# Kernel tuning notes

Hardware: AMD Instinct MI355X
Metric: run time of the kernel (lower is better)

The kernel has to match this reference:

```python
import jax, jax.numpy as jnp
import numpy as np

B, S, H = 8, 2048, 768      # batch, seq_len, hidden_size
N = 512                     # spans per example
MAXW = 30                   # max span width (length in [0, MAXW-1] -> width <= MAXW)


def setup_inputs() -> dict:
    key = jax.random.key(0)
    k1, k2, k3, k4 = jax.random.split(key, 4)
    embeddings = jax.random.normal(k1, (B, S, H), dtype=jnp.float32)
    starts = jax.random.randint(k2, (B, N), 0, S - MAXW)          # span starts
    lengths = jax.random.randint(k3, (B, N), 0, MAXW)             # end = start + length
    w = jax.random.normal(k4, (H, 1), dtype=jnp.float32) * 0.02   # nn.Linear(hidden, 1) weight (transposed)
    b = jnp.zeros((1,), dtype=jnp.float32)                        # linear bias
    return {"embeddings": embeddings, "w": w, "b": b, "starts": starts, "lengths": lengths}


def reference(embeddings, w, b, starts, lengths):
    # Vectorized ragged span pooling: gather up to MAXW tokens per span,
    # masked softmax over attention scores, then concat [start, end, attn].
    ends = starts + lengths                                  # inclusive end index
    offs = jnp.arange(MAXW)                                  # (W,)
    positions = starts[..., None] + offs                     # (B, N, W)
    mask = offs[None, None, :] <= lengths[..., None]         # (B, N, W) valid-token mask

    gather = jax.vmap(lambda e, p: e[p])                     # per-example gather
    span_emb = gather(embeddings, positions)                 # (B, N, W, H)

    scores = span_emb @ w + b                                # (B, N, W, 1)
    scores = jnp.where(mask[..., None], scores, -jnp.inf)
    attn_w = jax.nn.softmax(scores, axis=2)                  # masked softmax over span width
    attn_out = jnp.sum(attn_w * span_emb, axis=2)            # (B, N, H)

    start_emb = gather(embeddings, starts)                   # (B, N, H)
    end_emb = gather(embeddings, ends)                       # (B, N, H)
    return jnp.concatenate([start_emb, end_emb, attn_out], axis=-1)  # (B, N, 3H)
```

## Files before the change

### kernel.cpp

```cpp
#include <hip/hip_runtime.h>
#include <hip/hip_bf16.h>
#include <math.h>

#define BB 8
#define SS 2048
#define HH 768
#define NN 512
#define MAXW 30

__global__ __launch_bounds__(256) void sort_spans_kernel(
    const int* __restrict__ starts,
    int*       __restrict__ order)
{
    const int b   = blockIdx.x;
    const int tid = threadIdx.x;
    __shared__ int hist[SS];
    __shared__ int wsum[4];

    for (int i = tid; i < SS; i += 256) hist[i] = 0;
    __syncthreads();

    const int* st = starts + b * NN;
    for (int n = tid; n < NN; n += 256) atomicAdd(&hist[st[n]], 1);
    __syncthreads();

    const int base = tid * 8;
    int cnt[8]; int s = 0;
    #pragma unroll
    for (int k = 0; k < 8; ++k) { cnt[k] = hist[base + k]; s += cnt[k]; }

    const int lane = tid & 63, wv = tid >> 6;
    int v = s;
    #pragma unroll
    for (int off = 1; off < 64; off <<= 1) {
        int u = __shfl_up(v, off);
        if (lane >= off) v += u;
    }
    if (lane == 63) wsum[wv] = v;
    __syncthreads();
    int wbase = 0;
    #pragma unroll
    for (int k = 0; k < 4; ++k) wbase += (k < wv) ? wsum[k] : 0;

    int excl = wbase + v - s;
    #pragma unroll
    for (int k = 0; k < 8; ++k) { int c = cnt[k]; hist[base + k] = excl; excl += c; }
    __syncthreads();

    for (int n = tid; n < NN; n += 256) {
        int pos = atomicAdd(&hist[st[n]], 1);
        order[b * NN + pos] = n;
    }
}

__global__ __launch_bounds__(256) void span_fused_kernel(
    const float* __restrict__ emb,
    const float* __restrict__ w,
    const float* __restrict__ bias,
    const int*   __restrict__ starts,
    const int*   __restrict__ lengths,
    const int*   __restrict__ order,
    float*       __restrict__ out)
{
    const int tid  = threadIdx.x;
    const int wv   = tid >> 6;
    const int lane = tid & 63;
    const int bi   = blockIdx.x & 7;
    const int rank = ((int)blockIdx.x >> 3) * 4 + wv;
    const int n    = order ? order[bi * NN + rank] : rank;
    const int span = bi * NN + n;

    const int start = starts[span];
    const int len   = lengths[span];

    const float* ebase = emb + (size_t)bi * SS * HH + (size_t)start * HH;
    const int h0 = lane * 4;
    float* orow = out + (size_t)span * (3 * HH);

    const float4 w0 = *reinterpret_cast<const float4*>(w + h0);
    const float4 w1 = *reinterpret_cast<const float4*>(w + h0 + 256);
    const float4 w2 = *reinterpret_cast<const float4*>(w + h0 + 512);
    const float bb = bias[0];

    float m = -INFINITY, ssum = 0.f;
    float4 a0 = make_float4(0.f, 0.f, 0.f, 0.f), a1 = a0, a2 = a0;

    const float* row = ebase;
    float4 v0 = *reinterpret_cast<const float4*>(row + h0);
    float4 v1 = *reinterpret_cast<const float4*>(row + h0 + 256);
    float4 v2 = *reinterpret_cast<const float4*>(row + h0 + 512);

    for (int t = 0; t <= len; ++t) {
        float4 n0, n1, n2;
        if (t < len) {
            const float* nr = row + HH;
            n0 = *reinterpret_cast<const float4*>(nr + h0);
            n1 = *reinterpret_cast<const float4*>(nr + h0 + 256);
            n2 = *reinterpret_cast<const float4*>(nr + h0 + 512);
        }

        float d = v0.x * w0.x + v0.y * w0.y + v0.z * w0.z + v0.w * w0.w
                + v1.x * w1.x + v1.y * w1.y + v1.z * w1.z + v1.w * w1.w
                + v2.x * w2.x + v2.y * w2.y + v2.z * w2.z + v2.w * w2.w;
        #pragma unroll
        for (int off = 32; off; off >>= 1) d += __shfl_xor(d, off);
        d += bb;

        if (d > m) {
            const float c = __expf(m - d);
            ssum *= c;
            a0.x *= c; a0.y *= c; a0.z *= c; a0.w *= c;
            a1.x *= c; a1.y *= c; a1.z *= c; a1.w *= c;
            a2.x *= c; a2.y *= c; a2.z *= c; a2.w *= c;
            m = d;
        }
        const float pt = __expf(d - m);
        ssum += pt;
        a0.x += pt * v0.x; a0.y += pt * v0.y; a0.z += pt * v0.z; a0.w += pt * v0.w;
        a1.x += pt * v1.x; a1.y += pt * v1.y; a1.z += pt * v1.z; a1.w += pt * v1.w;
        a2.x += pt * v2.x; a2.y += pt * v2.y; a2.z += pt * v2.z; a2.w += pt * v2.w;

        if (t == 0) {
            *reinterpret_cast<float4*>(orow + h0)       = v0;
            *reinterpret_cast<float4*>(orow + h0 + 256) = v1;
            *reinterpret_cast<float4*>(orow + h0 + 512) = v2;
        }
        if (t == len) {
            *reinterpret_cast<float4*>(orow + HH + h0)       = v0;
            *reinterpret_cast<float4*>(orow + HH + h0 + 256) = v1;
            *reinterpret_cast<float4*>(orow + HH + h0 + 512) = v2;
        }

        v0 = n0; v1 = n1; v2 = n2;
        row += HH;
    }

    const float inv = 1.f / ssum;
    a0.x *= inv; a0.y *= inv; a0.z *= inv; a0.w *= inv;
    a1.x *= inv; a1.y *= inv; a1.z *= inv; a1.w *= inv;
    a2.x *= inv; a2.y *= inv; a2.z *= inv; a2.w *= inv;
    *reinterpret_cast<float4*>(orow + 2 * HH + h0)       = a0;
    *reinterpret_cast<float4*>(orow + 2 * HH + h0 + 256) = a1;
    *reinterpret_cast<float4*>(orow + 2 * HH + h0 + 512) = a2;
}

extern "C" void kernel_launch(void* const* d_in, const int* in_sizes, int n_in,
                              void* d_out, int out_size, void* d_ws, size_t ws_size,
                              hipStream_t stream) {
    const float* emb     = (const float*)d_in[0];
    const float* w       = (const float*)d_in[1];
    const float* bias    = (const float*)d_in[2];
    const int*   starts  = (const int*)d_in[3];
    const int*   lengths = (const int*)d_in[4];
    float*       out     = (float*)d_out;

    int* order = nullptr;
    if (ws_size >= (size_t)(BB * NN * sizeof(int))) {
        order = (int*)d_ws;
        sort_spans_kernel<<<dim3(BB), dim3(256), 0, stream>>>(starts, order);
    }

    span_fused_kernel<<<dim3(BB * NN / 4), dim3(256), 0, stream>>>(
        emb, w, bias, starts, lengths, order, out);
}
```

Measured before the change: 31.79 us.

## Share token rows across 8 sorted spans via double-buffered LDS chunks

Each 512-thread block now handles 8 start-sorted spans. It loads the union token window cooperatively in chunks of 8 rows into double-buffered shared memory, computing each row's score once. Each wave then runs the online softmax for its own span using the shared rows and scores. The aim is to remove redundant global loads and dot products for overlapping spans, at the cost of block-wide barriers, LDS traffic and possible loads of tokens no span in the block needs when the spans are spread apart.

New measurement: 36.76 us. +15.6%, slower.

```diff
diff --git a/kernel.cpp b/kernel.cpp
--- a/kernel.cpp
+++ b/kernel.cpp
@@ -7,6 +7,8 @@
 #define HH 768
 #define NN 512
 #define MAXW 30
+#define SPW 8
+#define CH  8
 
 __global__ __launch_bounds__(256) void sort_spans_kernel(
     const int* __restrict__ starts,
@@ -53,7 +55,7 @@
     }
 }
 
-__global__ __launch_bounds__(256) void span_fused_kernel(
+__global__ __launch_bounds__(512, 4) void span_block_kernel(
     const float* __restrict__ emb,
     const float* __restrict__ w,
     const float* __restrict__ bias,
@@ -66,73 +68,117 @@
     const int wv   = tid >> 6;
     const int lane = tid & 63;
     const int bi   = blockIdx.x & 7;
-    const int rank = ((int)blockIdx.x >> 3) * 4 + wv;
+    const int g    = (int)blockIdx.x >> 3;
+    const int rank = g * SPW + wv;
     const int n    = order ? order[bi * NN + rank] : rank;
     const int span = bi * NN + n;
 
     const int start = starts[span];
     const int len   = lengths[span];
-
-    const float* ebase = emb + (size_t)bi * SS * HH + (size_t)start * HH;
+    const int end   = start + len;
+
+    __shared__ float s_rows[2][CH][HH];
+    __shared__ float s_scr[2][CH];
+    __shared__ int   s_s[SPW], s_e[SPW];
+
+    if (lane == 0) { s_s[wv] = start; s_e[wv] = end; }
+    __syncthreads();
+    int wlo = s_s[0], whi = s_e[0];
+    #pragma unroll
+    for (int k = 1; k < SPW; ++k) { wlo = min(wlo, s_s[k]); whi = max(whi, s_e[k]); }
+
     const int h0 = lane * 4;
-    float* orow = out + (size_t)span * (3 * HH);
-
+    const float* ebase = emb + (size_t)bi * SS * HH;
     const float4 w0 = *reinterpret_cast<const float4*>(w + h0);
     const float4 w1 = *reinterpret_cast<const float4*>(w + h0 + 256);
     const float4 w2 = *reinterpret_cast<const float4*>(w + h0 + 512);
     const float bb = bias[0];
 
+    const int nch = (whi - wlo) / CH + 1;
+
+    auto produce = [&](int c) {
+        const int tok = wlo + c * CH + wv;
+        if (tok <= whi) {
+            const float* rp = ebase + (size_t)tok * HH + h0;
+            float4 v0 = *reinterpret_cast<const float4*>(rp);
+            float4 v1 = *reinterpret_cast<const float4*>(rp + 256);
+            float4 v2 = *reinterpret_cast<const float4*>(rp + 512);
+            float d = v0.x * w0.x + v0.y * w0.y + v0.z * w0.z + v0.w * w0.w
+                    + v1.x * w1.x + v1.y * w1.y + v1.z * w1.z + v1.w * w1.w
+                    + v2.x * w2.x + v2.y * w2.y + v2.z * w2.z + v2.w * w2.w;
+            #pragma unroll
+            for (int off = 32; off; off >>= 1) d += __shfl_xor(d, off);
+            float* dst = &s_rows[c & 1][wv][h0];
+            *reinterpret_cast<float4*>(dst)       = v0;
+            *reinterpret_cast<float4*>(dst + 256) = v1;
+            *reinterpret_cast<float4*>(dst + 512) = v2;
+            if (lane == 0) s_scr[c & 1][wv] = d + bb;
+        }
+    };
+
     float m = -INFINITY, ssum = 0.f;
     float4 a0 = make_float4(0.f, 0.f, 0.f, 0.f), a1 = a0, a2 = a0;
-
-    const float* row = ebase;
-    float4 v0 = *reinterpret_cast<const float4*>(row + h0);
-    float4 v1 = *reinterpret_cast<const float4*>(row + h0 + 256);
-    float4 v2 = *reinterpret_cast<const float4*>(row + h0 + 512);
-
-    for (int t = 0; t <= len; ++t) {
-        float4 n0, n1, n2;
-        if (t < len) {
-            const float* nr = row + HH;
-            n0 = *reinterpret_cast<const float4*>(nr + h0);
-            n1 = *reinterpret_cast<const float4*>(nr + h0 + 256);
-            n2 = *reinterpret_cast<const float4*>(nr + h0 + 512);
+    float* orow = out + (size_t)span * (3 * HH);
+
+    produce(0);
+    __syncthreads();
+
+    for (int c = 0; c < nch; ++c) {
+        if (c + 1 < nch) produce(c + 1);
+
+        const int clo = wlo + c * CH;
+        const int t0  = max(clo, start);
+        const int t1  = min(clo + CH - 1, end);
+        const int buf = c & 1;
+
+        if (t0 <= t1) {
+            int j = t0 - clo;
+            float ds = s_scr[buf][j];
+            const float* rp0 = &s_rows[buf][j][h0];
+            float4 v0 = *reinterpret_cast<const float4*>(rp0);
+            float4 v1 = *reinterpret_cast<const float4*>(rp0 + 256);
+            float4 v2 = *reinterpret_cast<const float4*>(rp0 + 512);
+
+            for (int t = t0; t <= t1; ++t) {
+                float nds = 0.f; float4 n0, n1, n2;
+                if (t < t1) {
+                    const int j2 = t + 1 - clo;
+                    nds = s_scr[buf][j2];
+                    const float* np = &s_rows[buf][j2][h0];
+                    n0 = *reinterpret_cast<const float4*>(np);
+                    n1 = *reinterpret_cast<const float4*>(np + 256);
+                    n2 = *reinterpret_cast<const float4*>(np + 512);
+                }
+
+                if (ds > m) {
+                    const float cc = __expf(m - ds);
+                    ssum *= cc;
+                    a0.x *= cc; a0.y *= cc; a0.z *= cc; a0.w *= cc;
+                    a1.x *= cc; a1.y *= cc; a1.z *= cc; a1.w *= cc;
+                    a2.x *= cc; a2.y *= cc; a2.z *= cc; a2.w *= cc;
+                    m = ds;
+                }
+                const float pt = __expf(ds - m);
+                ssum += pt;
+                a0.x += pt * v0.x; a0.y += pt * v0.y; a0.z += pt * v0.z; a0.w += pt * v0.w;
+                a1.x += pt * v1.x; a1.y += pt * v1.y; a1.z += pt * v1.z; a1.w += pt * v1.w;
+                a2.x += pt * v2.x; a2.y += pt * v2.y; a2.z += pt * v2.z; a2.w += pt * v2.w;
+
+                if (t == start) {
+                    *reinterpret_cast<float4*>(orow + h0)       = v0;
+                    *reinterpret_cast<float4*>(orow + h0 + 256) = v1;
+                    *reinterpret_cast<float4*>(orow + h0 + 512) = v2;
+                }
+                if (t == end) {
+                    *reinterpret_cast<float4*>(orow + HH + h0)       = v0;
+                    *reinterpret_cast<float4*>(orow + HH + h0 + 256) = v1;
+                    *reinterpret_cast<float4*>(orow + HH + h0 + 512) = v2;
+                }
+
+                ds = nds; v0 = n0; v1 = n1; v2 = n2;
+            }
         }
-
-        float d = v0.x * w0.x + v0.y * w0.y + v0.z * w0.z + v0.w * w0.w
-                + v1.x * w1.x + v1.y * w1.y + v1.z * w1.z + v1.w * w1.w
-                + v2.x * w2.x + v2.y * w2.y + v2.z * w2.z + v2.w * w2.w;
-        #pragma unroll
-        for (int off = 32; off; off >>= 1) d += __shfl_xor(d, off);
-        d += bb;
-
-        if (d > m) {
-            const float c = __expf(m - d);
-            ssum *= c;
-            a0.x *= c; a0.y *= c; a0.z *= c; a0.w *= c;
-            a1.x *= c; a1.y *= c; a1.z *= c; a1.w *= c;
-            a2.x *= c; a2.y *= c; a2.z *= c; a2.w *= c;
-            m = d;
-        }
-        const float pt = __expf(d - m);
-        ssum += pt;
-        a0.x += pt * v0.x; a0.y += pt * v0.y; a0.z += pt * v0.z; a0.w += pt * v0.w;
-        a1.x += pt * v1.x; a1.y += pt * v1.y; a1.z += pt * v1.z; a1.w += pt * v1.w;
-        a2.x += pt * v2.x; a2.y += pt * v2.y; a2.z += pt * v2.z; a2.w += pt * v2.w;
-
-        if (t == 0) {
-            *reinterpret_cast<float4*>(orow + h0)       = v0;
-            *reinterpret_cast<float4*>(orow + h0 + 256) = v1;
-            *reinterpret_cast<float4*>(orow + h0 + 512) = v2;
-        }
-        if (t == len) {
-            *reinterpret_cast<float4*>(orow + HH + h0)       = v0;
-            *reinterpret_cast<float4*>(orow + HH + h0 + 256) = v1;
-            *reinterpret_cast<float4*>(orow + HH + h0 + 512) = v2;
-        }
-
-        v0 = n0; v1 = n1; v2 = n2;
-        row += HH;
+        __syncthreads();
     }
 
     const float inv = 1.f / ssum;
@@ -160,6 +206,6 @@
         sort_spans_kernel<<<dim3(BB), dim3(256), 0, stream>>>(starts, order);
     }
 
-    span_fused_kernel<<<dim3(BB * NN / 4), dim3(256), 0, stream>>>(
+    span_block_kernel<<<dim3(BB * NN / SPW), dim3(512), 0, stream>>>(
         emb, w, bias, starts, lengths, order, out);
 }
```

## Split each span's token loop across two wavefronts and merge softmax partials in LDS

Applied to the files above, without the earlier changes.

Each span is now handled by two wavefronts instead of one. Each wavefront runs an online softmax over half of the span's tokens, and the two partial maxima, sums and accumulators are merged through shared memory. This halves the serial dependent-load chain per wave, which should cut latency and tail imbalance caused by long spans. In exchange the grid doubles, two block barriers and LDS traffic are added, and a launch-bounds occupancy hint is set.

After: 33.19 us. +4.4%, slower.

```diff
diff --git a/kernel.cpp b/kernel.cpp
--- a/kernel.cpp
+++ b/kernel.cpp
@@ -53,7 +53,7 @@
     }
 }
 
-__global__ __launch_bounds__(256) void span_fused_kernel(
+__global__ __launch_bounds__(256, 6) void span_split_kernel(
     const float* __restrict__ emb,
     const float* __restrict__ w,
     const float* __restrict__ bias,
@@ -65,13 +65,21 @@
     const int tid  = threadIdx.x;
     const int wv   = tid >> 6;
     const int lane = tid & 63;
+    const int p    = wv >> 1;
+    const int hf   = wv & 1;
+
     const int bi   = blockIdx.x & 7;
-    const int rank = ((int)blockIdx.x >> 3) * 4 + wv;
+    const int g    = (int)blockIdx.x >> 3;
+    const int rank = g * 2 + p;
     const int n    = order ? order[bi * NN + rank] : rank;
     const int span = bi * NN + n;
 
     const int start = starts[span];
     const int len   = lengths[span];
+    const int cntT  = len + 1;
+    const int mid   = (cntT + 1) >> 1;
+    const int t_lo  = hf ? mid : 0;
+    const int t_hi  = hf ? len : (mid - 1);
 
     const float* ebase = emb + (size_t)bi * SS * HH + (size_t)start * HH;
     const int h0 = lane * 4;
@@ -85,63 +93,97 @@
     float m = -INFINITY, ssum = 0.f;
     float4 a0 = make_float4(0.f, 0.f, 0.f, 0.f), a1 = a0, a2 = a0;
 
-    const float* row = ebase;
-    float4 v0 = *reinterpret_cast<const float4*>(row + h0);
-    float4 v1 = *reinterpret_cast<const float4*>(row + h0 + 256);
-    float4 v2 = *reinterpret_cast<const float4*>(row + h0 + 512);
-
-    for (int t = 0; t <= len; ++t) {
-        float4 n0, n1, n2;
-        if (t < len) {
-            const float* nr = row + HH;
-            n0 = *reinterpret_cast<const float4*>(nr + h0);
-            n1 = *reinterpret_cast<const float4*>(nr + h0 + 256);
-            n2 = *reinterpret_cast<const float4*>(nr + h0 + 512);
+    if (t_lo <= t_hi) {
+        const float* row = ebase + (size_t)t_lo * HH;
+        float4 v0 = *reinterpret_cast<const float4*>(row + h0);
+        float4 v1 = *reinterpret_cast<const float4*>(row + h0 + 256);
+        float4 v2 = *reinterpret_cast<const float4*>(row + h0 + 512);
+
+        for (int t = t_lo; t <= t_hi; ++t) {
+            float4 n0, n1, n2;
+            if (t < t_hi) {
+                const float* nr = row + HH;
+                n0 = *reinterpret_cast<const float4*>(nr + h0);
+                n1 = *reinterpret_cast<const float4*>(nr + h0 + 256);
+                n2 = *reinterpret_cast<const float4*>(nr + h0 + 512);
+            }
+
+            float d = v0.x * w0.x + v0.y * w0.y + v0.z * w0.z + v0.w * w0.w
+                    + v1.x * w1.x + v1.y * w1.y + v1.z * w1.z + v1.w * w1.w
+                    + v2.x * w2.x + v2.y * w2.y + v2.z * w2.z + v2.w * w2.w;
+            #pragma unroll
+            for (int off = 32; off; off >>= 1) d += __shfl_xor(d, off);
+            d += bb;
+
+            if (d > m) {
+                const float c = __expf(m - d);
+                ssum *= c;
+                a0.x *= c; a0.y *= c; a0.z *= c; a0.w *= c;
+                a1.x *= c; a1.y *= c; a1.z *= c; a1.w *= c;
+                a2.x *= c; a2.y *= c; a2.z *= c; a2.w *= c;
+                m = d;
+            }
+            const float pt = __expf(d - m);
+            ssum += pt;
+            a0.x += pt * v0.x; a0.y += pt * v0.y; a0.z += pt * v0.z; a0.w += pt * v0.w;
+            a1.x += pt * v1.x; a1.y += pt * v1.y; a1.z += pt * v1.z; a1.w += pt * v1.w;
+            a2.x += pt * v2.x; a2.y += pt * v2.y; a2.z += pt * v2.z; a2.w += pt * v2.w;
+
+            if (t == 0) {
+                *reinterpret_cast<float4*>(orow + h0)       = v0;
+                *reinterpret_cast<float4*>(orow + h0 + 256) = v1;
+                *reinterpret_cast<float4*>(orow + h0 + 512) = v2;
+            }
+            if (t == len) {
+                *reinterpret_cast<float4*>(orow + HH + h0)       = v0;
+                *reinterpret_cast<float4*>(orow + HH + h0 + 256) = v1;
+                *reinterpret_cast<float4*>(orow + HH + h0 + 512) = v2;
+            }
+
+            v0 = n0; v1 = n1; v2 = n2;
+            row += HH;
         }
-
-        float d = v0.x * w0.x + v0.y * w0.y + v0.z * w0.z + v0.w * w0.w
-                + v1.x * w1.x + v1.y * w1.y + v1.z * w1.z + v1.w * w1.w
-                + v2.x * w2.x + v2.y * w2.y + v2.z * w2.z + v2.w * w2.w;
-        #pragma unroll
-        for (int off = 32; off; off >>= 1) d += __shfl_xor(d, off);
-        d += bb;
-
-        if (d > m) {
-            const float c = __expf(m - d);
-            ssum *= c;
-            a0.x *= c; a0.y *= c; a0.z *= c; a0.w *= c;
-            a1.x *= c; a1.y *= c; a1.z *= c; a1.w *= c;
-            a2.x *= c; a2.y *= c; a2.z *= c; a2.w *= c;
-            m = d;
-        }
-        const float pt = __expf(d - m);
-        ssum += pt;
-        a0.x += pt * v0.x; a0.y += pt * v0.y; a0.z += pt * v0.z; a0.w += pt * v0.w;
-        a1.x += pt * v1.x; a1.y += pt * v1.y; a1.z += pt * v1.z; a1.w += pt * v1.w;
-        a2.x += pt * v2.x; a2.y += pt * v2.y; a2.z += pt * v2.z; a2.w += pt * v2.w;
-
-        if (t == 0) {
-            *reinterpret_cast<float4*>(orow + h0)       = v0;
-            *reinterpret_cast<float4*>(orow + h0 + 256) = v1;
-            *reinterpret_cast<float4*>(orow + h0 + 512) = v2;
-        }
-        if (t == len) {
-            *reinterpret_cast<float4*>(orow + HH + h0)       = v0;
-            *reinterpret_cast<float4*>(orow + HH + h0 + 256) = v1;
-            *reinterpret_cast<float4*>(orow + HH + h0 + 512) = v2;
-        }
-
-        v0 = n0; v1 = n1; v2 = n2;
-        row += HH;
-    }
-
-    const float inv = 1.f / ssum;
-    a0.x *= inv; a0.y *= inv; a0.z *= inv; a0.w *= inv;
-    a1.x *= inv; a1.y *= inv; a1.z *= inv; a1.w *= inv;
-    a2.x *= inv; a2.y *= inv; a2.z *= inv; a2.w *= inv;
-    *reinterpret_cast<float4*>(orow + 2 * HH + h0)       = a0;
-    *reinterpret_cast<float4*>(orow + 2 * HH + h0 + 256) = a1;
-    *reinterpret_cast<float4*>(orow + 2 * HH + h0 + 512) = a2;
+    }
+
+    __shared__ float s_m[2][2];
+    __shared__ float s_sum[2][2];
+    __shared__ float s_acc[2][HH];
+
+    s_m[p][hf] = m;
+    __syncthreads();
+    const float M = fmaxf(s_m[p][0], s_m[p][1]);
+    const float c = __expf(m - M);
+    ssum *= c;
+    a0.x *= c; a0.y *= c; a0.z *= c; a0.w *= c;
+    a1.x *= c; a1.y *= c; a1.z *= c; a1.w *= c;
+    a2.x *= c; a2.y *= c; a2.z *= c; a2.w *= c;
+
+    if (hf == 1) {
+        s_sum[p][1] = ssum;
+        float* dst = &s_acc[p][h0];
+        *reinterpret_cast<float4*>(dst)       = a0;
+        *reinterpret_cast<float4*>(dst + 256) = a1;
+        *reinterpret_cast<float4*>(dst + 512) = a2;
+    }
+    __syncthreads();
+
+    if (hf == 0) {
+        const float total = ssum + s_sum[p][1];
+        const float inv = 1.f / total;
+        const float* src = &s_acc[p][h0];
+        float4 b0 = *reinterpret_cast<const float4*>(src);
+        float4 b1 = *reinterpret_cast<const float4*>(src + 256);
+        float4 b2 = *reinterpret_cast<const float4*>(src + 512);
+        a0.x = (a0.x + b0.x) * inv; a0.y = (a0.y + b0.y) * inv;
+        a0.z = (a0.z + b0.z) * inv; a0.w = (a0.w + b0.w) * inv;
+        a1.x = (a1.x + b1.x) * inv; a1.y = (a1.y + b1.y) * inv;
+        a1.z = (a1.z + b1.z) * inv; a1.w = (a1.w + b1.w) * inv;
+        a2.x = (a2.x + b2.x) * inv; a2.y = (a2.y + b2.y) * inv;
+        a2.z = (a2.z + b2.z) * inv; a2.w = (a2.w + b2.w) * inv;
+        *reinterpret_cast<float4*>(orow + 2 * HH + h0)       = a0;
+        *reinterpret_cast<float4*>(orow + 2 * HH + h0 + 256) = a1;
+        *reinterpret_cast<float4*>(orow + 2 * HH + h0 + 512) = a2;
+    }
 }
 
 extern "C" void kernel_launch(void* const* d_in, const int* in_sizes, int n_in,
@@ -160,6 +202,6 @@
         sort_spans_kernel<<<dim3(BB), dim3(256), 0, stream>>>(starts, order);
     }
 
-    span_fused_kernel<<<dim3(BB * NN / 4), dim3(256), 0, stream>>>(
+    span_split_kernel<<<dim3(BB * NN / 2), dim3(256), 0, stream>>>(
         emb, w, bias, starts, lengths, order, out);
 }
```

## Process pairs of start-sorted spans per wavefront over their union token range

Applied to the files above, without the earlier changes.

Each wavefront now handles two adjacent spans from the start-sorted order. It walks the union of their token ranges once, computing each token's attention score a single time and feeding it into two separate online-softmax accumulators. Prefetch depth grows to two rows ahead. This is meant to remove duplicated row loads and dot-product reductions for overlapping spans. The cost is half as many wavefronts for latency hiding, more registers, and extra iterations where the two spans do not overlap.

Result: slower. 35.51 us (+11.7%).

```diff
diff --git a/kernel.cpp b/kernel.cpp
--- a/kernel.cpp
+++ b/kernel.cpp
@@ -53,7 +53,7 @@
     }
 }
 
-__global__ __launch_bounds__(256) void span_fused_kernel(
+__global__ __launch_bounds__(256) void span_pair_kernel(
     const float* __restrict__ emb,
     const float* __restrict__ w,
     const float* __restrict__ bias,
@@ -66,82 +66,127 @@
     const int wv   = tid >> 6;
     const int lane = tid & 63;
     const int bi   = blockIdx.x & 7;
-    const int rank = ((int)blockIdx.x >> 3) * 4 + wv;
-    const int n    = order ? order[bi * NN + rank] : rank;
-    const int span = bi * NN + n;
-
-    const int start = starts[span];
-    const int len   = lengths[span];
-
-    const float* ebase = emb + (size_t)bi * SS * HH + (size_t)start * HH;
+    const int g    = (int)blockIdx.x >> 3;
+    const int pr   = g * 4 + wv;
+    const int rkA  = pr * 2, rkB = rkA + 1;
+    const int nA   = order ? order[bi * NN + rkA] : rkA;
+    const int nB   = order ? order[bi * NN + rkB] : rkB;
+    const int spanA = bi * NN + nA;
+    const int spanB = bi * NN + nB;
+
+    const int startA = starts[spanA], lenA = lengths[spanA], endA = startA + lenA;
+    const int startB = starts[spanB], lenB = lengths[spanB], endB = startB + lenB;
+    const int lo = min(startA, startB);
+    const int hi = max(endA, endB);
+
+    const float* ebase = emb + (size_t)bi * SS * HH;
     const int h0 = lane * 4;
-    float* orow = out + (size_t)span * (3 * HH);
+    float* orA = out + (size_t)spanA * (3 * HH);
+    float* orB = out + (size_t)spanB * (3 * HH);
 
     const float4 w0 = *reinterpret_cast<const float4*>(w + h0);
     const float4 w1 = *reinterpret_cast<const float4*>(w + h0 + 256);
     const float4 w2 = *reinterpret_cast<const float4*>(w + h0 + 512);
     const float bb = bias[0];
 
-    float m = -INFINITY, ssum = 0.f;
-    float4 a0 = make_float4(0.f, 0.f, 0.f, 0.f), a1 = a0, a2 = a0;
-
-    const float* row = ebase;
-    float4 v0 = *reinterpret_cast<const float4*>(row + h0);
-    float4 v1 = *reinterpret_cast<const float4*>(row + h0 + 256);
-    float4 v2 = *reinterpret_cast<const float4*>(row + h0 + 512);
-
-    for (int t = 0; t <= len; ++t) {
-        float4 n0, n1, n2;
-        if (t < len) {
-            const float* nr = row + HH;
-            n0 = *reinterpret_cast<const float4*>(nr + h0);
-            n1 = *reinterpret_cast<const float4*>(nr + h0 + 256);
-            n2 = *reinterpret_cast<const float4*>(nr + h0 + 512);
-        }
-
-        float d = v0.x * w0.x + v0.y * w0.y + v0.z * w0.z + v0.w * w0.w
-                + v1.x * w1.x + v1.y * w1.y + v1.z * w1.z + v1.w * w1.w
-                + v2.x * w2.x + v2.y * w2.y + v2.z * w2.z + v2.w * w2.w;
+    float mA = -INFINITY, sA = 0.f;
+    float4 aA0 = make_float4(0.f,0.f,0.f,0.f), aA1 = aA0, aA2 = aA0;
+    float mB = -INFINITY, sB = 0.f;
+    float4 aB0 = aA0, aB1 = aA0, aB2 = aA0;
+
+    const float* p0 = ebase + (size_t)lo * HH + h0;
+    float4 c0 = *reinterpret_cast<const float4*>(p0);
+    float4 c1 = *reinterpret_cast<const float4*>(p0 + 256);
+    float4 c2 = *reinterpret_cast<const float4*>(p0 + 512);
+    const float* p1 = ebase + (size_t)min(lo + 1, hi) * HH + h0;
+    float4 x0 = *reinterpret_cast<const float4*>(p1);
+    float4 x1 = *reinterpret_cast<const float4*>(p1 + 256);
+    float4 x2 = *reinterpret_cast<const float4*>(p1 + 512);
+
+    for (int t = lo; t <= hi; ++t) {
+        const float* p2 = ebase + (size_t)min(t + 2, hi) * HH + h0;
+        float4 y0 = *reinterpret_cast<const float4*>(p2);
+        float4 y1 = *reinterpret_cast<const float4*>(p2 + 256);
+        float4 y2 = *reinterpret_cast<const float4*>(p2 + 512);
+
+        float d = c0.x * w0.x + c0.y * w0.y + c0.z * w0.z + c0.w * w0.w
+                + c1.x * w1.x + c1.y * w1.y + c1.z * w1.z + c1.w * w1.w
+                + c2.x * w2.x + c2.y * w2.y + c2.z * w2.z + c2.w * w2.w;
         #pragma unroll
         for (int off = 32; off; off >>= 1) d += __shfl_xor(d, off);
         d += bb;
 
-        if (d > m) {
-            const float c = __expf(m - d);
-            ssum *= c;
-            a0.x *= c; a0.y *= c; a0.z *= c; a0.w *= c;
-            a1.x *= c; a1.y *= c; a1.z *= c; a1.w *= c;
-            a2.x *= c; a2.y *= c; a2.z *= c; a2.w *= c;
-            m = d;
+        if (t >= startA && t <= endA) {
+            if (d > mA) {
+                const float c = __expf(mA - d);
+                sA *= c;
+                aA0.x *= c; aA0.y *= c; aA0.z *= c; aA0.w *= c;
+                aA1.x *= c; aA1.y *= c; aA1.z *= c; aA1.w *= c;
+                aA2.x *= c; aA2.y *= c; aA2.z *= c; aA2.w *= c;
+                mA = d;
+            }
+            const float pt = __expf(d - mA);
+            sA += pt;
+            aA0.x += pt * c0.x; aA0.y += pt * c0.y; aA0.z += pt * c0.z; aA0.w += pt * c0.w;
+            aA1.x += pt * c1.x; aA1.y += pt * c1.y; aA1.z += pt * c1.z; aA1.w += pt * c1.w;
+            aA2.x += pt * c2.x; aA2.y += pt * c2.y; aA2.z += pt * c2.z; aA2.w += pt * c2.w;
+            if (t == startA) {
+                *reinterpret_cast<float4*>(orA + h0)       = c0;
+                *reinterpret_cast<float4*>(orA + h0 + 256) = c1;
+                *reinterpret_cast<float4*>(orA + h0 + 512) = c2;
+            }
+            if (t == endA) {
+                *reinterpret_cast<float4*>(orA + HH + h0)       = c0;
+                *reinterpret_cast<float4*>(orA + HH + h0 + 256) = c1;
+                *reinterpret_cast<float4*>(orA + HH + h0 + 512) = c2;
+            }
         }
-        const float pt = __expf(d - m);
-        ssum += pt;
-        a0.x += pt * v0.x; a0.y += pt * v0.y; a0.z += pt * v0.z; a0.w += pt * v0.w;
-        a1.x += pt * v1.x; a1.y += pt * v1.y; a1.z += pt * v1.z; a1.w += pt * v1.w;
-        a2.x += pt * v2.x; a2.y += pt * v2.y; a2.z += pt * v2.z; a2.w += pt * v2.w;
-
-        if (t == 0) {
-            *reinterpret_cast<float4*>(orow + h0)       = v0;
-            *reinterpret_cast<float4*>(orow + h0 + 256) = v1;
-            *reinterpret_cast<float4*>(orow + h0 + 512) = v2;
+
+        if (t >= startB && t <= endB) {
+            if (d > mB) {
+                const float c = __expf(mB - d);
+                sB *= c;
+                aB0.x *= c; aB0.y *= c; aB0.z *= c; aB0.w *= c;
+                aB1.x *= c; aB1.y *= c; aB1.z *= c; aB1.w *= c;
+                aB2.x *= c; aB2.y *= c; aB2.z *= c; aB2.w *= c;
+                mB = d;
+            }
+            const float pt = __expf(d - mB);
+            sB += pt;
+            aB0.x += pt * c0.x; aB0.y += pt * c0.y; aB0.z += pt * c0.z; aB0.w += pt * c0.w;
+            aB1.x += pt * c1.x; aB1.y += pt * c1.y; aB1.z += pt * c1.z; aB1.w += pt * c1.w;
+            aB2.x += pt * c2.x; aB2.y += pt * c2.y; aB2.z += pt * c2.z; aB2.w += pt * c2.w;
+            if (t == startB) {
+                *reinterpret_cast<float4*>(orB + h0)       = c0;
+                *reinterpret_cast<float4*>(orB + h0 + 256) = c1;
+                *reinterpret_cast<float4*>(orB + h0 + 512) = c2;
+            }
+            if (t == endB) {
+                *reinterpret_cast<float4*>(orB + HH + h0)       = c0;
+                *reinterpret_cast<float4*>(orB + HH + h0 + 256) = c1;
+                *reinterpret_cast<float4*>(orB + HH + h0 + 512) = c2;
+            }
         }
-        if (t == len) {
-            *reinterpret_cast<float4*>(orow + HH + h0)       = v0;
-            *reinterpret_cast<float4*>(orow + HH + h0 + 256) = v1;
-            *reinterpret_cast<float4*>(orow + HH + h0 + 512) = v2;
-        }
-
-        v0 = n0; v1 = n1; v2 = n2;
-        row += HH;
-    }
-
-    const float inv = 1.f / ssum;
-    a0.x *= inv; a0.y *= inv; a0.z *= inv; a0.w *= inv;
-    a1.x *= inv; a1.y *= inv; a1.z *= inv; a1.w *= inv;
-    a2.x *= inv; a2.y *= inv; a2.z *= inv; a2.w *= inv;
-    *reinterpret_cast<float4*>(orow + 2 * HH + h0)       = a0;
-    *reinterpret_cast<float4*>(orow + 2 * HH + h0 + 256) = a1;
-    *reinterpret_cast<float4*>(orow + 2 * HH + h0 + 512) = a2;
+
+        c0 = x0; c1 = x1; c2 = x2;
+        x0 = y0; x1 = y1; x2 = y2;
+    }
+
+    const float invA = 1.f / sA;
+    aA0.x *= invA; aA0.y *= invA; aA0.z *= invA; aA0.w *= invA;
+    aA1.x *= invA; aA1.y *= invA; aA1.z *= invA; aA1.w *= invA;
+    aA2.x *= invA; aA2.y *= invA; aA2.z *= invA; aA2.w *= invA;
+    *reinterpret_cast<float4*>(orA + 2 * HH + h0)       = aA0;
+    *reinterpret_cast<float4*>(orA + 2 * HH + h0 + 256) = aA1;
+    *reinterpret_cast<float4*>(orA + 2 * HH + h0 + 512) = aA2;
+
+    const float invB = 1.f / sB;
+    aB0.x *= invB; aB0.y *= invB; aB0.z *= invB; aB0.w *= invB;
+    aB1.x *= invB; aB1.y *= invB; aB1.z *= invB; aB1.w *= invB;
+    aB2.x *= invB; aB2.y *= invB; aB2.z *= invB; aB2.w *= invB;
+    *reinterpret_cast<float4*>(orB + 2 * HH + h0)       = aB0;
+    *reinterpret_cast<float4*>(orB + 2 * HH + h0 + 256) = aB1;
+    *reinterpret_cast<float4*>(orB + 2 * HH + h0 + 512) = aB2;
 }
 
 extern "C" void kernel_launch(void* const* d_in, const int* in_sizes, int n_in,
@@ -160,6 +205,6 @@
         sort_spans_kernel<<<dim3(BB), dim3(256), 0, stream>>>(starts, order);
     }
 
-    span_fused_kernel<<<dim3(BB * NN / 4), dim3(256), 0, stream>>>(
+    span_pair_kernel<<<dim3(BB * NN / 8), dim3(256), 0, stream>>>(
         emb, w, bias, starts, lengths, order, out);
 }
```
